# Kernel optimization log

Hardware: AMD Instinct MI355X
Metric: run time of the kernel (lower is better)

## Reference

```python
import jax, jax.numpy as jnp
import numpy as np

H = 4096        # hidden_size
NH = 32         # num query heads
NKV = 8         # num kv heads
HD = H // NH    # head_dim = 128
T_PREV = 16383  # cached tokens; new token makes T = 16384
BASE = 10000.0


def _rope(x, pos):
    # x: [heads, head_dim]; interleaved even/odd RoPE at a single position
    d = x.shape[-1]
    inv_freq = 1.0 / (BASE ** (jnp.arange(0, d, 2, dtype=jnp.float32) / d))
    f = pos * inv_freq                      # [d/2]
    c, s = jnp.cos(f), jnp.sin(f)
    xe, xo = x[..., 0::2], x[..., 1::2]
    out = jnp.stack([xe * c - xo * s, xe * s + xo * c], axis=-1)
    return out.reshape(x.shape)


def setup_inputs() -> dict:
    key = jax.random.key(0)
    ks = jax.random.split(key, 7)
    w = 0.02  # weight scale for numerical stability
    return {
        "hidden": jax.random.normal(ks[0], (H,), jnp.float32),
        "k_cache": jax.random.normal(ks[1], (T_PREV, NKV, HD), jnp.float32),
        "v_cache": jax.random.normal(ks[2], (T_PREV, NKV, HD), jnp.float32),
        "Wq": jax.random.normal(ks[3], (H, H), jnp.float32) * w,
        "Wk": jax.random.normal(ks[4], (NKV * HD, H), jnp.float32) * w,
        "Wv": jax.random.normal(ks[5], (NKV * HD, H), jnp.float32) * w,
        "Wo": jax.random.normal(ks[6], (H, H), jnp.float32) * w,
        "position_id": T_PREV,
    }


def reference(hidden, k_cache, v_cache, Wq, Wk, Wv, Wo, position_id):
    pos = jnp.float32(position_id)
    # projections (nn.Linear: y = W @ x), single token
    q = (Wq @ hidden).reshape(NH, HD)
    k = (Wk @ hidden).reshape(NKV, HD)
    v = (Wv @ hidden).reshape(NKV, HD)
    # inline RoPE on new q and k
    q = _rope(q, pos)
    k = _rope(k, pos)
    # contiguous KV including the new token
    k_all = jnp.concatenate([k_cache, k[None]], axis=0)   # [T, NKV, HD]
    v_all = jnp.concatenate([v_cache, v[None]], axis=0)
    # GQA: repeat KV heads to match query heads
    rep = NH // NKV
    k_all = jnp.repeat(k_all, rep, axis=1)                 # [T, NH, HD]
    v_all = jnp.repeat(v_all, rep, axis=1)
    # single-query attention
    scores = jnp.einsum('hd,thd->ht', q, k_all) / jnp.sqrt(jnp.float32(HD))
    attn = jax.nn.softmax(scores, axis=-1)                 # [NH, T]
    ctx = jnp.einsum('ht,thd->hd', attn, v_all)            # [NH, HD]
    # combine heads + output projection
    return Wo @ ctx.reshape(H)
```

## Files before the change

### kernel.cpp

```cpp
#include <hip/hip_runtime.h>
#include <math.h>

#define NH 32
#define NKV 8
#define HD 128
#define HDIM 4096
#define KVDIM 1024
#define TPREV 16383
#define NCHUNK 64
#define CHUNK 256

#define OFF_Q 0
#define OFF_K 4096
#define OFF_V 5120
#define OFF_PART 6144
#define PART_STRIDE 130
#define OFF_CTX (OFF_PART + NH * NCHUNK * PART_STRIDE)

__device__ __forceinline__ float wave_reduce_sum(float v) {
#pragma unroll
  for (int m = 32; m >= 1; m >>= 1) v += __shfl_xor(v, m, 64);
  return v;
}

__global__ __launch_bounds__(256) void qkv_rope_kernel(
    const float* __restrict__ Wq, const float* __restrict__ Wk,
    const float* __restrict__ Wv, const float* __restrict__ hidden,
    const int* __restrict__ pos_p, float* __restrict__ ws) {
  int r0 = blockIdx.x * 2;
  const float* W;
  int wr;
  if (r0 < HDIM) {
    W = Wq; wr = r0;
  } else if (r0 < HDIM + KVDIM) {
    W = Wk; wr = r0 - HDIM;
  } else {
    W = Wv; wr = r0 - HDIM - KVDIM;
  }
  const float4* w0 = (const float4*)(W + (size_t)wr * HDIM);
  const float4* w1 = (const float4*)(W + (size_t)(wr + 1) * HDIM);
  const float4* h4 = (const float4*)hidden;
  int t = threadIdx.x;
  float s0 = 0.f, s1 = 0.f;
#pragma unroll
  for (int k = 0; k < 4; ++k) {
    int idx = t + 256 * k;
    float4 b = h4[idx];
    float4 a0 = w0[idx];
    float4 a1 = w1[idx];
    s0 += a0.x * b.x + a0.y * b.y + a0.z * b.z + a0.w * b.w;
    s1 += a1.x * b.x + a1.y * b.y + a1.z * b.z + a1.w * b.w;
  }
  s0 = wave_reduce_sum(s0);
  s1 = wave_reduce_sum(s1);
  __shared__ float redA[4], redB[4];
  if ((t & 63) == 0) {
    redA[t >> 6] = s0;
    redB[t >> 6] = s1;
  }
  __syncthreads();
  if (t == 0) {
    float S0 = redA[0] + redA[1] + redA[2] + redA[3];
    float S1 = redB[0] + redB[1] + redB[2] + redB[3];
    if (r0 < HDIM + KVDIM) {
      int j = (r0 & (HD - 1)) >> 1;
      double f = (double)(*pos_p) * pow(10000.0, -(double)j / 64.0);
      float c = (float)cos(f), sn = (float)sin(f);
      ws[r0] = S0 * c - S1 * sn;
      ws[r0 + 1] = S0 * sn + S1 * c;
    } else {
      ws[r0] = S0;
      ws[r0 + 1] = S1;
    }
  }
}

__global__ __launch_bounds__(256) void attn_chunk_kernel(
    const float* __restrict__ k_cache, const float* __restrict__ v_cache,
    float* __restrict__ ws) {
  int g = blockIdx.x / NCHUNK;
  int c = blockIdx.x % NCHUNK;
  int t0 = c * CHUNK;
  int ntok = TPREV - t0;
  if (ntok > CHUNK) ntok = CHUNK;
  int tid = threadIdx.x;

  __shared__ float qs[4 * HD];
  __shared__ float sc[CHUNK * 5];
  __shared__ float wredm[4][4], wredl[4][4];
  __shared__ float mh[4], lh[4];

  for (int i = tid; i < 4 * HD; i += 256) qs[i] = ws[OFF_Q + (g * 4) * HD + i];
  __syncthreads();

  const float rscale = 0.08838834764831845f;
  int grp = tid >> 5, lane = tid & 31;

  for (int it = grp; it < CHUNK; it += 8) {
    int t = t0 + it;
    if (t < TPREV) {
      float4 kv = ((const float4*)(k_cache + (size_t)t * (NKV * HD) + g * HD))[lane];
      float4 q0 = ((const float4*)(qs + 0 * HD))[lane];
      float4 q1 = ((const float4*)(qs + 1 * HD))[lane];
      float4 q2 = ((const float4*)(qs + 2 * HD))[lane];
      float4 q3 = ((const float4*)(qs + 3 * HD))[lane];
      float s0 = kv.x * q0.x + kv.y * q0.y + kv.z * q0.z + kv.w * q0.w;
      float s1 = kv.x * q1.x + kv.y * q1.y + kv.z * q1.z + kv.w * q1.w;
      float s2 = kv.x * q2.x + kv.y * q2.y + kv.z * q2.z + kv.w * q2.w;
      float s3 = kv.x * q3.x + kv.y * q3.y + kv.z * q3.z + kv.w * q3.w;
#pragma unroll
      for (int m = 16; m >= 1; m >>= 1) {
        s0 += __shfl_xor(s0, m, 64);
        s1 += __shfl_xor(s1, m, 64);
        s2 += __shfl_xor(s2, m, 64);
        s3 += __shfl_xor(s3, m, 64);
      }
      if (lane == 0) {
        sc[it * 5 + 0] = s0 * rscale;
        sc[it * 5 + 1] = s1 * rscale;
        sc[it * 5 + 2] = s2 * rscale;
        sc[it * 5 + 3] = s3 * rscale;
      }
    } else {
      if (lane == 0) {
        sc[it * 5 + 0] = -1e30f;
        sc[it * 5 + 1] = -1e30f;
        sc[it * 5 + 2] = -1e30f;
        sc[it * 5 + 3] = -1e30f;
      }
    }
  }
  __syncthreads();

  float m0 = sc[tid * 5 + 0], m1 = sc[tid * 5 + 1];
  float m2 = sc[tid * 5 + 2], m3 = sc[tid * 5 + 3];
#pragma unroll
  for (int m = 32; m >= 1; m >>= 1) {
    m0 = fmaxf(m0, __shfl_xor(m0, m, 64));
    m1 = fmaxf(m1, __shfl_xor(m1, m, 64));
    m2 = fmaxf(m2, __shfl_xor(m2, m, 64));
    m3 = fmaxf(m3, __shfl_xor(m3, m, 64));
  }
  if ((tid & 63) == 0) {
    int w = tid >> 6;
    wredm[w][0] = m0; wredm[w][1] = m1; wredm[w][2] = m2; wredm[w][3] = m3;
  }
  __syncthreads();
  if (tid < 4)
    mh[tid] = fmaxf(fmaxf(wredm[0][tid], wredm[1][tid]),
                    fmaxf(wredm[2][tid], wredm[3][tid]));
  __syncthreads();

  float M0 = mh[0], M1 = mh[1], M2 = mh[2], M3 = mh[3];
  float e0 = expf(sc[tid * 5 + 0] - M0);
  float e1 = expf(sc[tid * 5 + 1] - M1);
  float e2 = expf(sc[tid * 5 + 2] - M2);
  float e3 = expf(sc[tid * 5 + 3] - M3);
  sc[tid * 5 + 0] = e0;
  sc[tid * 5 + 1] = e1;
  sc[tid * 5 + 2] = e2;
  sc[tid * 5 + 3] = e3;
  float l0 = wave_reduce_sum(e0);
  float l1 = wave_reduce_sum(e1);
  float l2 = wave_reduce_sum(e2);
  float l3 = wave_reduce_sum(e3);
  if ((tid & 63) == 0) {
    int w = tid >> 6;
    wredl[w][0] = l0; wredl[w][1] = l1; wredl[w][2] = l2; wredl[w][3] = l3;
  }
  __syncthreads();
  if (tid < 4)
    lh[tid] = wredl[0][tid] + wredl[1][tid] + wredl[2][tid] + wredl[3][tid];
  __syncthreads();

  int d = tid & (HD - 1);
  int h0 = tid >> 7;
  const float* vp = v_cache + (size_t)t0 * (NKV * HD) + g * HD + d;
  float a0 = 0.f, a1 = 0.f;
  for (int it = 0; it < ntok; ++it) {
    float v = vp[(size_t)it * (NKV * HD)];
    a0 = fmaf(sc[it * 5 + h0], v, a0);
    a1 = fmaf(sc[it * 5 + h0 + 2], v, a1);
  }
  float* part = ws + OFF_PART;
  part[(size_t)((g * 4 + h0) * NCHUNK + c) * PART_STRIDE + d] = a0;
  part[(size_t)((g * 4 + h0 + 2) * NCHUNK + c) * PART_STRIDE + d] = a1;
  if (tid < 4) {
    part[(size_t)((g * 4 + tid) * NCHUNK + c) * PART_STRIDE + 128] = mh[tid];
    part[(size_t)((g * 4 + tid) * NCHUNK + c) * PART_STRIDE + 129] = lh[tid];
  }
}

__global__ __launch_bounds__(128) void combine_kernel(float* __restrict__ ws) {
  int h = blockIdx.x;
  int g = h >> 2;
  int d = threadIdx.x;
  const float rscale = 0.08838834764831845f;

  __shared__ float red[HD];
  red[d] = ws[OFF_Q + h * HD + d] * ws[OFF_K + g * HD + d];
  __syncthreads();
#pragma unroll
  for (int s = 64; s >= 1; s >>= 1) {
    if (d < s) red[d] += red[d + s];
    __syncthreads();
  }
  float snew = red[0] * rscale;

  const float* ph = ws + OFF_PART + (size_t)h * NCHUNK * PART_STRIDE;
  float M = snew;
  for (int c = 0; c < NCHUNK; ++c) M = fmaxf(M, ph[c * PART_STRIDE + 128]);
  float en = expf(snew - M);
  float L = en;
  float acc = en * ws[OFF_V + g * HD + d];
  for (int c = 0; c < NCHUNK; ++c) {
    float w = expf(ph[c * PART_STRIDE + 128] - M);
    L += ph[c * PART_STRIDE + 129] * w;
    acc += ph[c * PART_STRIDE + d] * w;
  }
  ws[OFF_CTX + h * HD + d] = acc / L;
}

__global__ __launch_bounds__(256) void out_matvec_kernel(
    const float* __restrict__ Wo, const float* __restrict__ ws,
    float* __restrict__ out) {
  int r0 = blockIdx.x * 2;
  const float4* w0 = (const float4*)(Wo + (size_t)r0 * HDIM);
  const float4* w1 = (const float4*)(Wo + (size_t)(r0 + 1) * HDIM);
  const float4* x4 = (const float4*)(ws + OFF_CTX);
  int t = threadIdx.x;
  float s0 = 0.f, s1 = 0.f;
#pragma unroll
  for (int k = 0; k < 4; ++k) {
    int idx = t + 256 * k;
    float4 b = x4[idx];
    float4 a0 = w0[idx];
    float4 a1 = w1[idx];
    s0 += a0.x * b.x + a0.y * b.y + a0.z * b.z + a0.w * b.w;
    s1 += a1.x * b.x + a1.y * b.y + a1.z * b.z + a1.w * b.w;
  }
  s0 = wave_reduce_sum(s0);
  s1 = wave_reduce_sum(s1);
  __shared__ float redA[4], redB[4];
  if ((t & 63) == 0) {
    redA[t >> 6] = s0;
    redB[t >> 6] = s1;
  }
  __syncthreads();
  if (t == 0) {
    out[r0] = redA[0] + redA[1] + redA[2] + redA[3];
    out[r0 + 1] = redB[0] + redB[1] + redB[2] + redB[3];
  }
}

extern "C" void kernel_launch(void* const* d_in, const int* in_sizes, int n_in,
                              void* d_out, int out_size, void* d_ws,
                              size_t ws_size, hipStream_t stream) {
  const float* hidden = (const float*)d_in[0];
  const float* k_cache = (const float*)d_in[1];
  const float* v_cache = (const float*)d_in[2];
  const float* Wq = (const float*)d_in[3];
  const float* Wk = (const float*)d_in[4];
  const float* Wv = (const float*)d_in[5];
  const float* Wo = (const float*)d_in[6];
  const int* pos = (const int*)d_in[7];
  float* out = (float*)d_out;
  float* ws = (float*)d_ws;

  qkv_rope_kernel<<<(HDIM + KVDIM + KVDIM) / 2, 256, 0, stream>>>(
      Wq, Wk, Wv, hidden, pos, ws);
  attn_chunk_kernel<<<NKV * NCHUNK, 256, 0, stream>>>(k_cache, v_cache, ws);
  combine_kernel<<<NH, 128, 0, stream>>>(ws);
  out_matvec_kernel<<<HDIM / 2, 256, 0, stream>>>(Wo, ws, out);
}
```

Measured before the change: 305.8 us.

## Vectorize PV loop, halve chunk size, one row per wave in matvecs, parallelize combine

The attention kernel's P·V stage now loads V as float4 per lane, with 8 token groups each covering all four heads, then reduces through shared memory. This replaces the scalar, token-serial loop with its long dependent load chain. Chunks are halved to 128 tokens, doubling the block count for more parallelism at the cost of more partials to combine. The QKV and output matvecs now assign one row per wavefront, which drops a shared-memory reduction. The combine kernel computes the max and sum with parallel reductions instead of serial loops.

```diff
diff --git a/kernel.cpp b/kernel.cpp
--- a/kernel.cpp
+++ b/kernel.cpp
@@ -7,8 +7,8 @@
 #define HDIM 4096
 #define KVDIM 1024
 #define TPREV 16383
-#define NCHUNK 64
-#define CHUNK 256
+#define NCHUNK 128
+#define CHUNK 128
 
 #define OFF_Q 0
 #define OFF_K 4096
@@ -22,46 +22,43 @@
   for (int m = 32; m >= 1; m >>= 1) v += __shfl_xor(v, m, 64);
   return v;
 }
+__device__ __forceinline__ float wave_reduce_max(float v) {
+#pragma unroll
+  for (int m = 32; m >= 1; m >>= 1) v = fmaxf(v, __shfl_xor(v, m, 64));
+  return v;
+}
 
 __global__ __launch_bounds__(256) void qkv_rope_kernel(
     const float* __restrict__ Wq, const float* __restrict__ Wk,
     const float* __restrict__ Wv, const float* __restrict__ hidden,
     const int* __restrict__ pos_p, float* __restrict__ ws) {
-  int r0 = blockIdx.x * 2;
+  int r = blockIdx.x * 4 + (threadIdx.x >> 6);
+  int lane = threadIdx.x & 63;
   const float* W;
   int wr;
-  if (r0 < HDIM) {
-    W = Wq; wr = r0;
-  } else if (r0 < HDIM + KVDIM) {
-    W = Wk; wr = r0 - HDIM;
+  if (r < HDIM) {
+    W = Wq; wr = r;
+  } else if (r < HDIM + KVDIM) {
+    W = Wk; wr = r - HDIM;
   } else {
-    W = Wv; wr = r0 - HDIM - KVDIM;
-  }
-  const float4* w0 = (const float4*)(W + (size_t)wr * HDIM);
-  const float4* w1 = (const float4*)(W + (size_t)(wr + 1) * HDIM);
+    W = Wv; wr = r - HDIM - KVDIM;
+  }
+  const float4* w4 = (const float4*)(W + (size_t)wr * HDIM);
   const float4* h4 = (const float4*)hidden;
-  int t = threadIdx.x;
-  float s0 = 0.f, s1 = 0.f;
-#pragma unroll
-  for (int k = 0; k < 4; ++k) {
-    int idx = t + 256 * k;
-    float4 b = h4[idx];
-    float4 a0 = w0[idx];
-    float4 a1 = w1[idx];
-    s0 += a0.x * b.x + a0.y * b.y + a0.z * b.z + a0.w * b.w;
-    s1 += a1.x * b.x + a1.y * b.y + a1.z * b.z + a1.w * b.w;
-  }
-  s0 = wave_reduce_sum(s0);
-  s1 = wave_reduce_sum(s1);
-  __shared__ float redA[4], redB[4];
-  if ((t & 63) == 0) {
-    redA[t >> 6] = s0;
-    redB[t >> 6] = s1;
-  }
-  __syncthreads();
-  if (t == 0) {
-    float S0 = redA[0] + redA[1] + redA[2] + redA[3];
-    float S1 = redB[0] + redB[1] + redB[2] + redB[3];
+  float s = 0.f;
+#pragma unroll
+  for (int i = 0; i < 16; ++i) {
+    float4 a = w4[lane + 64 * i];
+    float4 b = h4[lane + 64 * i];
+    s += a.x * b.x + a.y * b.y + a.z * b.z + a.w * b.w;
+  }
+  s = wave_reduce_sum(s);
+  __shared__ float rs[4];
+  if (lane == 0) rs[threadIdx.x >> 6] = s;
+  __syncthreads();
+  if (threadIdx.x < 2) {
+    int r0 = blockIdx.x * 4 + (int)threadIdx.x * 2;
+    float S0 = rs[threadIdx.x * 2], S1 = rs[threadIdx.x * 2 + 1];
     if (r0 < HDIM + KVDIM) {
       int j = (r0 & (HD - 1)) >> 1;
       double f = (double)(*pos_p) * pow(10000.0, -(double)j / 64.0);
@@ -78,19 +75,18 @@
 __global__ __launch_bounds__(256) void attn_chunk_kernel(
     const float* __restrict__ k_cache, const float* __restrict__ v_cache,
     float* __restrict__ ws) {
-  int g = blockIdx.x / NCHUNK;
-  int c = blockIdx.x % NCHUNK;
+  int g = blockIdx.x >> 7;
+  int c = blockIdx.x & 127;
   int t0 = c * CHUNK;
-  int ntok = TPREV - t0;
-  if (ntok > CHUNK) ntok = CHUNK;
   int tid = threadIdx.x;
 
   __shared__ float qs[4 * HD];
   __shared__ float sc[CHUNK * 5];
+  __shared__ float vacc[8][4][HD];
   __shared__ float wredm[4][4], wredl[4][4];
   __shared__ float mh[4], lh[4];
 
-  for (int i = tid; i < 4 * HD; i += 256) qs[i] = ws[OFF_Q + (g * 4) * HD + i];
+  for (int i = tid; i < 4 * HD; i += 256) qs[i] = ws[OFF_Q + g * 4 * HD + i];
   __syncthreads();
 
   const float rscale = 0.08838834764831845f;
@@ -99,7 +95,7 @@
   for (int it = grp; it < CHUNK; it += 8) {
     int t = t0 + it;
     if (t < TPREV) {
-      float4 kv = ((const float4*)(k_cache + (size_t)t * (NKV * HD) + g * HD))[lane];
+      float4 kv = ((const float4*)(k_cache + (size_t)t * KVDIM + g * HD))[lane];
       float4 q0 = ((const float4*)(qs + 0 * HD))[lane];
       float4 q1 = ((const float4*)(qs + 1 * HD))[lane];
       float4 q2 = ((const float4*)(qs + 2 * HD))[lane];
@@ -121,26 +117,22 @@
         sc[it * 5 + 2] = s2 * rscale;
         sc[it * 5 + 3] = s3 * rscale;
       }
-    } else {
-      if (lane == 0) {
-        sc[it * 5 + 0] = -1e30f;
-        sc[it * 5 + 1] = -1e30f;
-        sc[it * 5 + 2] = -1e30f;
-        sc[it * 5 + 3] = -1e30f;
-      }
+    } else if (lane == 0) {
+      sc[it * 5 + 0] = -1e30f;
+      sc[it * 5 + 1] = -1e30f;
+      sc[it * 5 + 2] = -1e30f;
+      sc[it * 5 + 3] = -1e30f;
     }
   }
   __syncthreads();
 
-  float m0 = sc[tid * 5 + 0], m1 = sc[tid * 5 + 1];
-  float m2 = sc[tid * 5 + 2], m3 = sc[tid * 5 + 3];
-#pragma unroll
-  for (int m = 32; m >= 1; m >>= 1) {
-    m0 = fmaxf(m0, __shfl_xor(m0, m, 64));
-    m1 = fmaxf(m1, __shfl_xor(m1, m, 64));
-    m2 = fmaxf(m2, __shfl_xor(m2, m, 64));
-    m3 = fmaxf(m3, __shfl_xor(m3, m, 64));
-  }
+  float m0 = -1e30f, m1 = -1e30f, m2 = -1e30f, m3 = -1e30f;
+  if (tid < CHUNK) {
+    m0 = sc[tid * 5 + 0]; m1 = sc[tid * 5 + 1];
+    m2 = sc[tid * 5 + 2]; m3 = sc[tid * 5 + 3];
+  }
+  m0 = wave_reduce_max(m0); m1 = wave_reduce_max(m1);
+  m2 = wave_reduce_max(m2); m3 = wave_reduce_max(m3);
   if ((tid & 63) == 0) {
     int w = tid >> 6;
     wredm[w][0] = m0; wredm[w][1] = m1; wredm[w][2] = m2; wredm[w][3] = m3;
@@ -152,14 +144,17 @@
   __syncthreads();
 
   float M0 = mh[0], M1 = mh[1], M2 = mh[2], M3 = mh[3];
-  float e0 = expf(sc[tid * 5 + 0] - M0);
-  float e1 = expf(sc[tid * 5 + 1] - M1);
-  float e2 = expf(sc[tid * 5 + 2] - M2);
-  float e3 = expf(sc[tid * 5 + 3] - M3);
-  sc[tid * 5 + 0] = e0;
-  sc[tid * 5 + 1] = e1;
-  sc[tid * 5 + 2] = e2;
-  sc[tid * 5 + 3] = e3;
+  float e0 = 0.f, e1 = 0.f, e2 = 0.f, e3 = 0.f;
+  if (tid < CHUNK) {
+    e0 = expf(sc[tid * 5 + 0] - M0);
+    e1 = expf(sc[tid * 5 + 1] - M1);
+    e2 = expf(sc[tid * 5 + 2] - M2);
+    e3 = expf(sc[tid * 5 + 3] - M3);
+    sc[tid * 5 + 0] = e0;
+    sc[tid * 5 + 1] = e1;
+    sc[tid * 5 + 2] = e2;
+    sc[tid * 5 + 3] = e3;
+  }
   float l0 = wave_reduce_sum(e0);
   float l1 = wave_reduce_sum(e1);
   float l2 = wave_reduce_sum(e2);
@@ -173,84 +168,120 @@
     lh[tid] = wredl[0][tid] + wredl[1][tid] + wredl[2][tid] + wredl[3][tid];
   __syncthreads();
 
-  int d = tid & (HD - 1);
-  int h0 = tid >> 7;
-  const float* vp = v_cache + (size_t)t0 * (NKV * HD) + g * HD + d;
-  float a0 = 0.f, a1 = 0.f;
-  for (int it = 0; it < ntok; ++it) {
-    float v = vp[(size_t)it * (NKV * HD)];
-    a0 = fmaf(sc[it * 5 + h0], v, a0);
-    a1 = fmaf(sc[it * 5 + h0 + 2], v, a1);
-  }
+  float4 a0 = {0, 0, 0, 0}, a1 = {0, 0, 0, 0}, a2 = {0, 0, 0, 0},
+         a3 = {0, 0, 0, 0};
+  for (int it = grp; it < CHUNK; it += 8) {
+    int t = t0 + it;
+    if (t < TPREV) {
+      float4 v = ((const float4*)(v_cache + (size_t)t * KVDIM + g * HD))[lane];
+      float p0 = sc[it * 5 + 0], p1 = sc[it * 5 + 1];
+      float p2 = sc[it * 5 + 2], p3 = sc[it * 5 + 3];
+      a0.x = fmaf(p0, v.x, a0.x); a0.y = fmaf(p0, v.y, a0.y);
+      a0.z = fmaf(p0, v.z, a0.z); a0.w = fmaf(p0, v.w, a0.w);
+      a1.x = fmaf(p1, v.x, a1.x); a1.y = fmaf(p1, v.y, a1.y);
+      a1.z = fmaf(p1, v.z, a1.z); a1.w = fmaf(p1, v.w, a1.w);
+      a2.x = fmaf(p2, v.x, a2.x); a2.y = fmaf(p2, v.y, a2.y);
+      a2.z = fmaf(p2, v.z, a2.z); a2.w = fmaf(p2, v.w, a2.w);
+      a3.x = fmaf(p3, v.x, a3.x); a3.y = fmaf(p3, v.y, a3.y);
+      a3.z = fmaf(p3, v.z, a3.z); a3.w = fmaf(p3, v.w, a3.w);
+    }
+  }
+  ((float4*)&vacc[grp][0][0])[lane] = a0;
+  ((float4*)&vacc[grp][1][0])[lane] = a1;
+  ((float4*)&vacc[grp][2][0])[lane] = a2;
+  ((float4*)&vacc[grp][3][0])[lane] = a3;
+  __syncthreads();
+
   float* part = ws + OFF_PART;
-  part[(size_t)((g * 4 + h0) * NCHUNK + c) * PART_STRIDE + d] = a0;
-  part[(size_t)((g * 4 + h0 + 2) * NCHUNK + c) * PART_STRIDE + d] = a1;
+#pragma unroll
+  for (int rep = 0; rep < 2; ++rep) {
+    int p = tid + rep * 256;
+    int h = p >> 7, d = p & 127;
+    float s = 0.f;
+#pragma unroll
+    for (int g2 = 0; g2 < 8; ++g2) s += vacc[g2][h][d];
+    part[(size_t)((g * 4 + h) * NCHUNK + c) * PART_STRIDE + d] = s;
+  }
   if (tid < 4) {
     part[(size_t)((g * 4 + tid) * NCHUNK + c) * PART_STRIDE + 128] = mh[tid];
     part[(size_t)((g * 4 + tid) * NCHUNK + c) * PART_STRIDE + 129] = lh[tid];
   }
 }
 
-__global__ __launch_bounds__(128) void combine_kernel(float* __restrict__ ws) {
+__global__ __launch_bounds__(256) void combine_kernel(float* __restrict__ ws) {
   int h = blockIdx.x;
   int g = h >> 2;
-  int d = threadIdx.x;
+  int tid = threadIdx.x;
   const float rscale = 0.08838834764831845f;
+  const float* ph = ws + OFF_PART + (size_t)h * NCHUNK * PART_STRIDE;
 
   __shared__ float red[HD];
-  red[d] = ws[OFF_Q + h * HD + d] * ws[OFF_K + g * HD + d];
-  __syncthreads();
-#pragma unroll
-  for (int s = 64; s >= 1; s >>= 1) {
-    if (d < s) red[d] += red[d + s];
+  __shared__ float wexp[NCHUNK];
+  __shared__ float wm[4], wl[4];
+  __shared__ float acc2[HD];
+
+  if (tid < HD) red[tid] = ws[OFF_Q + h * HD + tid] * ws[OFF_K + g * HD + tid];
+  __syncthreads();
+#pragma unroll
+  for (int s2 = 64; s2 >= 1; s2 >>= 1) {
+    if (tid < s2 && tid + s2 < HD) red[tid] += red[tid + s2];
     __syncthreads();
   }
   float snew = red[0] * rscale;
 
-  const float* ph = ws + OFF_PART + (size_t)h * NCHUNK * PART_STRIDE;
-  float M = snew;
-  for (int c = 0; c < NCHUNK; ++c) M = fmaxf(M, ph[c * PART_STRIDE + 128]);
+  float mloc = -1e30f;
+  if (tid < NCHUNK) {
+    mloc = ph[tid * PART_STRIDE + 128];
+    wexp[tid] = mloc;
+  }
+  float mm = wave_reduce_max(fmaxf(mloc, snew));
+  if ((tid & 63) == 0) wm[tid >> 6] = mm;
+  __syncthreads();
+  float M = fmaxf(fmaxf(wm[0], wm[1]), fmaxf(wm[2], wm[3]));
+
+  float lpart = 0.f;
+  if (tid < NCHUNK) {
+    float w = expf(wexp[tid] - M);
+    lpart = ph[tid * PART_STRIDE + 129] * w;
+    wexp[tid] = w;
+  }
+  float lsum = wave_reduce_sum(lpart);
+  if ((tid & 63) == 0) wl[tid >> 6] = lsum;
+  __syncthreads();
   float en = expf(snew - M);
-  float L = en;
-  float acc = en * ws[OFF_V + g * HD + d];
-  for (int c = 0; c < NCHUNK; ++c) {
-    float w = expf(ph[c * PART_STRIDE + 128] - M);
-    L += ph[c * PART_STRIDE + 129] * w;
-    acc += ph[c * PART_STRIDE + d] * w;
-  }
-  ws[OFF_CTX + h * HD + d] = acc / L;
+  float L = wl[0] + wl[1] + wl[2] + wl[3] + en;
+
+  int half = tid >> 7, d = tid & 127;
+  float acc = 0.f;
+  int cbeg = half * 64;
+#pragma unroll 4
+  for (int c2 = cbeg; c2 < cbeg + 64; ++c2)
+    acc = fmaf(ph[(size_t)c2 * PART_STRIDE + d], wexp[c2], acc);
+  if (half == 0) acc2[d] = acc;
+  __syncthreads();
+  if (half == 1) acc2[d] += acc;
+  __syncthreads();
+  if (tid < HD)
+    ws[OFF_CTX + h * HD + tid] =
+        (acc2[tid] + en * ws[OFF_V + g * HD + tid]) / L;
 }
 
 __global__ __launch_bounds__(256) void out_matvec_kernel(
     const float* __restrict__ Wo, const float* __restrict__ ws,
     float* __restrict__ out) {
-  int r0 = blockIdx.x * 2;
-  const float4* w0 = (const float4*)(Wo + (size_t)r0 * HDIM);
-  const float4* w1 = (const float4*)(Wo + (size_t)(r0 + 1) * HDIM);
+  int r = blockIdx.x * 4 + (threadIdx.x >> 6);
+  int lane = threadIdx.x & 63;
+  const float4* w4 = (const float4*)(Wo + (size_t)r * HDIM);
   const float4* x4 = (const float4*)(ws + OFF_CTX);
-  int t = threadIdx.x;
-  float s0 = 0.f, s1 = 0.f;
-#pragma unroll
-  for (int k = 0; k < 4; ++k) {
-    int idx = t + 256 * k;
-    float4 b = x4[idx];
-    float4 a0 = w0[idx];
-    float4 a1 = w1[idx];
-    s0 += a0.x * b.x + a0.y * b.y + a0.z * b.z + a0.w * b.w;
-    s1 += a1.x * b.x + a1.y * b.y + a1.z * b.z + a1.w * b.w;
-  }
-  s0 = wave_reduce_sum(s0);
-  s1 = wave_reduce_sum(s1);
-  __shared__ float redA[4], redB[4];
-  if ((t & 63) == 0) {
-    redA[t >> 6] = s0;
-    redB[t >> 6] = s1;
-  }
-  __syncthreads();
-  if (t == 0) {
-    out[r0] = redA[0] + redA[1] + redA[2] + redA[3];
-    out[r0 + 1] = redB[0] + redB[1] + redB[2] + redB[3];
-  }
+  float s = 0.f;
+#pragma unroll
+  for (int i = 0; i < 16; ++i) {
+    float4 a = w4[lane + 64 * i];
+    float4 b = x4[lane + 64 * i];
+    s += a.x * b.x + a.y * b.y + a.z * b.z + a.w * b.w;
+  }
+  s = wave_reduce_sum(s);
+  if (lane == 0) out[r] = s;
 }
 
 extern "C" void kernel_launch(void* const* d_in, const int* in_sizes, int n_in,
@@ -267,9 +298,9 @@
   float* out = (float*)d_out;
   float* ws = (float*)d_ws;
 
-  qkv_rope_kernel<<<(HDIM + KVDIM + KVDIM) / 2, 256, 0, stream>>>(
-      Wq, Wk, Wv, hidden, pos, ws);
+  qkv_rope_kernel<<<(HDIM + 2 * KVDIM) / 4, 256, 0, stream>>>(Wq, Wk, Wv,
+                                                              hidden, pos, ws);
   attn_chunk_kernel<<<NKV * NCHUNK, 256, 0, stream>>>(k_cache, v_cache, ws);
-  combine_kernel<<<NH, 128, 0, stream>>>(ws);
-  out_matvec_kernel<<<HDIM / 2, 256, 0, stream>>>(Wo, ws, out);
-}
+  combine_kernel<<<NH, 256, 0, stream>>>(ws);
+  out_matvec_kernel<<<HDIM / 4, 256, 0, stream>>>(Wo, ws, out);
+}
```

Result: faster. 290.7 us (-4.9%).
